# Optimization experiments

Hardware: AMD Instinct MI355X
Metric: run time of the kernel (lower is better)

The kernel has to match this reference:

```python
import jax, jax.numpy as jnp
import numpy as np

# dims: B batch, T spikes, X/Y output grid, IN input neurons (weights rows), H hidden neurons
B, T, X, Y = 16, 128, 16, 16
IN_DIM, H_DIM = 256, 64


def setup_inputs() -> dict:
    key = jax.random.key(0)
    k1, k2, k3, k4, k5 = jax.random.split(key, 5)
    inp = {}
    # input only determines batch size in the custom forward (used by backward in torch)
    inp["input"] = jax.random.uniform(k1, (B, IN_DIM, X, Y), jnp.float32) + 0.01
    inp["spikes"] = jax.random.randint(k2, (B, T, X, Y), 0, IN_DIM)
    inp["epsilon_xy"] = jax.random.uniform(k3, (IN_DIM, X, Y), jnp.float32) * 0.1 + 0.01
    inp["epsilon_t_0"] = jax.random.uniform(k4, (T,), jnp.float32) * 0.5 + 0.5
    inp["weights"] = jax.random.uniform(k5, (IN_DIM, H_DIM), jnp.float32) + 1e-3
    inp["h_initial"] = jnp.ones((H_DIM,), jnp.float32) / H_DIM
    inp["forgetting_offset"] = jnp.ones((1,), jnp.float32)
    return inp


def _sbs_hdynamics(spikes, epsilon_xy, epsilon_t_0, weights, h_initial, fo):
    # spikes: [B,T,X,Y] int; weights: [IN,H]; epsilon_xy: [IN,X,Y]; h_initial: [H]
    b, t, x, y = spikes.shape
    h = weights.shape[1]
    xg = jnp.arange(x)[None, :, None]  # broadcast index grids for [B,X,Y] gathers
    yg = jnp.arange(y)[None, None, :]
    fo_per_neuron = fo / h
    h0 = jnp.broadcast_to(h_initial, (b, x, y, h)).astype(weights.dtype)

    def step(h_state, inp):
        sp, eps_t = inp                      # sp: [B,X,Y], eps_t: scalar
        w = weights[sp]                      # [B,X,Y,H] gather of weight rows
        eps = epsilon_xy[sp, xg, yg] * eps_t # [B,X,Y] per-pixel/spike epsilon
        h_temp = h_state * w                 # [B,X,Y,H]
        s = h_temp.sum(axis=-1)              # [B,X,Y]
        safe_s = jnp.where(s > 1e-10, s, 1.0)
        scale = (eps / safe_s)[..., None]
        # h <- (h + eps*h*w/ (h.w) + eps*fo/H) / (1 + eps*(1+fo))  (fo=0 reduces to h/(1+eps))
        upd = (h_state + scale * h_temp + (eps * fo_per_neuron)[..., None]) / (
            1.0 + (eps * (1.0 + fo))[..., None]
        )
        h_new = jnp.where((s > 1e-10)[..., None], upd, h_state)
        return h_new, None

    spikes_t = jnp.transpose(spikes, (1, 0, 2, 3))  # [T,B,X,Y]
    h_final, _ = jax.lax.scan(step, h0, (spikes_t, epsilon_t_0))
    return jnp.transpose(h_final, (0, 3, 1, 2))  # [B,H,X,Y]


def reference(input, spikes, epsilon_xy, epsilon_t_0, weights, h_initial, forgetting_offset):
    fo = forgetting_offset[0]
    return _sbs_hdynamics(spikes, epsilon_xy, epsilon_t_0, weights, h_initial, fo)
```

## Files before the change

### kernel.cpp

```cpp
#include <hip/hip_runtime.h>

#define BB      16
#define TT      128
#define XDIM    16
#define YDIM    16
#define IN_DIM  256
#define H_DIM   64
#define XY      (XDIM*YDIM)


#define DPP_ADD(v, ctrl)                                                      \
    v += __int_as_float(__builtin_amdgcn_update_dpp(                          \
        0, __float_as_int(v), (ctrl), 0xf, 0xf, true))

#define STEP(W, RD, ERD)                                                      \
    {                                                                         \
        const float ht0 = h.x * (W).x;                                        \
        const float ht1 = h.y * (W).y;                                        \
        const float ht2 = h.z * (W).z;                                        \
        const float ht3 = h.w * (W).w;                                        \
        float r = (ht0 + ht1) + (ht2 + ht3);                                  \
        const float erdf = (ERD) * fo_h;                                      \
        const float eht0 = (ERD) * ht0;                                       \
        const float eht1 = (ERD) * ht1;                                       \
        const float eht2 = (ERD) * ht2;                                       \
        const float eht3 = (ERD) * ht3;                                       \
        const float t30 = fmaf(h.x, (RD), erdf);                              \
        const float t31 = fmaf(h.y, (RD), erdf);                              \
        const float t32 = fmaf(h.z, (RD), erdf);                              \
        const float t33 = fmaf(h.w, (RD), erdf);                              \
        DPP_ADD(r, 0xB1);                                 \
        DPP_ADD(r, 0x4E);                    \
        DPP_ADD(r, 0x124);                                     \
        DPP_ADD(r, 0x128);                 \
        const float rs = __builtin_amdgcn_rcpf(r);  \
        h.x = fmaf(rs, eht0, t30);                                            \
        h.y = fmaf(rs, eht1, t31);                                            \
        h.z = fmaf(rs, eht2, t32);                                            \
        h.w = fmaf(rs, eht3, t33);                                            \
    }

__global__ __launch_bounds__(256) void sbs_scan_kernel(
    const int*   __restrict__ spikes,
    const float* __restrict__ eps_xy,
    const float* __restrict__ eps_t,
    const float* __restrict__ weights,
    const float* __restrict__ h_init,
    const float* __restrict__ fo_ptr,
    float*       __restrict__ out)
{
    __shared__ int4   s_spk4[YDIM][TT / 4 + 1];
    __shared__ float4 s_P4[YDIM][TT / 2 + 1];
    __shared__ float  s_out[YDIM][H_DIM + 1];

    const int tid = threadIdx.x;
    const int bi  = blockIdx.x;
    const int b   = bi >> 4;
    const int x   = bi & 15;

    int spv[8];
    #pragma unroll
    for (int k = 0; k < 8; ++k) {
        const int idx = tid + k * 256;
        const int t = idx >> 4, yy = idx & 15;
        const int sp = spikes[(b * TT + t) * XY + x * YDIM + yy];
        spv[k] = sp;
        ((int*)s_spk4[yy])[t] = sp;
    }

    const float fo   = fo_ptr[0];
    const float fo1  = 1.0f + fo;
    const float fo_h = fo * (1.0f / (float)H_DIM);

    #pragma unroll
    for (int k = 0; k < 8; ++k) {
        const int idx = tid + k * 256;
        const int t = idx >> 4, yy = idx & 15;
        const float eps = eps_xy[spv[k] * XY + x * YDIM + yy] * eps_t[t];
        const float den = fmaf(eps, fo1, 1.0f);
        float rd = __builtin_amdgcn_rcpf(den);
        rd = fmaf(rd, fmaf(-den, rd, 1.0f), rd);
        ((float2*)s_P4[yy])[t] = make_float2(rd, eps * rd);
    }
    __syncthreads();

    const int wave = tid >> 6;
    const int lane = tid & 63;
    const int row  = lane >> 4;
    const int il   = lane & 15;
    const int y    = wave * 4 + row;

    const float4* __restrict__ w4 = (const float4*)weights;
    const int4*   __restrict__ Sy = s_spk4[y];
    const float4* __restrict__ Py = s_P4[y];

    float4 h = ((const float4*)h_init)[il];

    const int4 s0 = Sy[0];
    int4   sA  = Sy[1];
    int4   sB  = Sy[2];
    float4 wq0 = w4[s0.x * 16 + il];
    float4 wq1 = w4[s0.y * 16 + il];
    float4 wq2 = w4[s0.z * 16 + il];
    float4 wq3 = w4[s0.w * 16 + il];
    float4 PA0 = Py[0], PA1 = Py[1];
    float4 PB0 = Py[2], PB1 = Py[3];

    #pragma unroll 2
    for (int g = 0; g < TT / 4; ++g) {
        const int4   s_in  = Sy[(g + 3) & 31];
        const float4 p_in0 = Py[(2 * g + 4) & 63];
        const float4 p_in1 = Py[(2 * g + 5) & 63];
        const float4 wn0 = w4[sA.x * 16 + il];
        const float4 wn1 = w4[sA.y * 16 + il];
        const float4 wn2 = w4[sA.z * 16 + il];
        const float4 wn3 = w4[sA.w * 16 + il];

        STEP(wq0, PA0.x, PA0.y);
        STEP(wq1, PA0.z, PA0.w);
        STEP(wq2, PA1.x, PA1.y);
        STEP(wq3, PA1.z, PA1.w);

        wq0 = wn0; wq1 = wn1; wq2 = wn2; wq3 = wn3;
        PA0 = PB0; PA1 = PB1; PB0 = p_in0; PB1 = p_in1;
        sA = sB; sB = s_in;
    }

    *(float4*)&s_out[y][4 * il] = h;
    __syncthreads();
    #pragma unroll
    for (int k = 0; k < 4; ++k) {
        const int idx = tid + k * 256;
        const int hh = idx >> 4, yy = idx & 15;
        out[b * (H_DIM * XY) + hh * XY + x * YDIM + yy] = s_out[yy][hh];
    }
}

extern "C" void kernel_launch(void* const* d_in, const int* in_sizes, int n_in,
                              void* d_out, int out_size, void* d_ws, size_t ws_size,
                              hipStream_t stream) {
    const int*   spikes  = (const int*)  d_in[1];
    const float* eps_xy  = (const float*)d_in[2];
    const float* eps_t   = (const float*)d_in[3];
    const float* weights = (const float*)d_in[4];
    const float* h_init  = (const float*)d_in[5];
    const float* fo_ptr  = (const float*)d_in[6];
    float*       out     = (float*)d_out;

    const int grid = BB * XDIM;
    sbs_scan_kernel<<<grid, 256, 0, stream>>>(
        spikes, eps_xy, eps_t, weights, h_init, fo_ptr, out);
}
```

Measured before the change: 76.96 us.

## Split each pixel's hidden vector across 32 lanes to double grid parallelism

Each pixel's 64-element hidden state is now spread over 32 lanes holding two values each, where before it was 16 lanes holding four. The per-step dot product therefore needs a cross-half-wave reduction, done with permlane32_swap when available and a shuffle otherwise. Each block now handles 8 pixels, so the grid doubles from 256 to 512 blocks. The aim is to cut the length of each lane's serial recurrence and fill more CUs on the MI355X, at the cost of an extra cross-lane reduction on the critical path of every timestep.

```diff
diff --git a/kernel.cpp b/kernel.cpp
--- a/kernel.cpp
+++ b/kernel.cpp
@@ -13,31 +13,34 @@
     v += __int_as_float(__builtin_amdgcn_update_dpp(                          \
         0, __float_as_int(v), (ctrl), 0xf, 0xf, true))
 
+__device__ __forceinline__ float cross_half_sum(float r) {
+#if __has_builtin(__builtin_amdgcn_permlane32_swap)
+    auto res = __builtin_amdgcn_permlane32_swap(
+        __float_as_uint(r), __float_as_uint(r), false, false);
+    return __uint_as_float(res[0]) + __uint_as_float(res[1]);
+#else
+    return r + __shfl_xor(r, 32);
+#endif
+}
+
 #define STEP(W, RD, ERD)                                                      \
     {                                                                         \
         const float ht0 = h.x * (W).x;                                        \
         const float ht1 = h.y * (W).y;                                        \
-        const float ht2 = h.z * (W).z;                                        \
-        const float ht3 = h.w * (W).w;                                        \
-        float r = (ht0 + ht1) + (ht2 + ht3);                                  \
+        float r = ht0 + ht1;                                                  \
         const float erdf = (ERD) * fo_h;                                      \
         const float eht0 = (ERD) * ht0;                                       \
         const float eht1 = (ERD) * ht1;                                       \
-        const float eht2 = (ERD) * ht2;                                       \
-        const float eht3 = (ERD) * ht3;                                       \
         const float t30 = fmaf(h.x, (RD), erdf);                              \
         const float t31 = fmaf(h.y, (RD), erdf);                              \
-        const float t32 = fmaf(h.z, (RD), erdf);                              \
-        const float t33 = fmaf(h.w, (RD), erdf);                              \
         DPP_ADD(r, 0xB1);                                 \
         DPP_ADD(r, 0x4E);                    \
         DPP_ADD(r, 0x124);                                     \
-        DPP_ADD(r, 0x128);                 \
-        const float rs = __builtin_amdgcn_rcpf(r);  \
+        DPP_ADD(r, 0x128);          \
+        const float s = cross_half_sum(r);        \
+        const float rs = __builtin_amdgcn_rcpf(s);  \
         h.x = fmaf(rs, eht0, t30);                                            \
         h.y = fmaf(rs, eht1, t31);                                            \
-        h.z = fmaf(rs, eht2, t32);                                            \
-        h.w = fmaf(rs, eht3, t33);                                            \
     }
 
 __global__ __launch_bounds__(256) void sbs_scan_kernel(
@@ -49,23 +52,24 @@
     const float* __restrict__ fo_ptr,
     float*       __restrict__ out)
 {
-    __shared__ int4   s_spk4[YDIM][TT / 4 + 1];
-    __shared__ float4 s_P4[YDIM][TT / 2 + 1];
-    __shared__ float  s_out[YDIM][H_DIM + 1];
+    __shared__ int4   s_spk4[8][TT / 4 + 1];
+    __shared__ float4 s_P4[8][TT / 2 + 1];
+    __shared__ float  s_out[8][H_DIM + 1];
 
     const int tid = threadIdx.x;
     const int bi  = blockIdx.x;
-    const int b   = bi >> 4;
-    const int x   = bi & 15;
+    const int b   = bi >> 5;
+    const int x   = (bi >> 1) & 15;
+    const int y0  = (bi & 1) * 8;
 
-    int spv[8];
+    int spv[4];
     #pragma unroll
-    for (int k = 0; k < 8; ++k) {
+    for (int k = 0; k < 4; ++k) {
         const int idx = tid + k * 256;
-        const int t = idx >> 4, yy = idx & 15;
-        const int sp = spikes[(b * TT + t) * XY + x * YDIM + yy];
+        const int t = idx >> 3, pb = idx & 7;
+        const int sp = spikes[(b * TT + t) * XY + x * YDIM + y0 + pb];
         spv[k] = sp;
-        ((int*)s_spk4[yy])[t] = sp;
+        ((int*)s_spk4[pb])[t] = sp;
     }
 
     const float fo   = fo_ptr[0];
@@ -73,36 +77,36 @@
     const float fo_h = fo * (1.0f / (float)H_DIM);
 
     #pragma unroll
-    for (int k = 0; k < 8; ++k) {
+    for (int k = 0; k < 4; ++k) {
         const int idx = tid + k * 256;
-        const int t = idx >> 4, yy = idx & 15;
-        const float eps = eps_xy[spv[k] * XY + x * YDIM + yy] * eps_t[t];
+        const int t = idx >> 3, pb = idx & 7;
+        const float eps = eps_xy[spv[k] * XY + x * YDIM + y0 + pb] * eps_t[t];
         const float den = fmaf(eps, fo1, 1.0f);
         float rd = __builtin_amdgcn_rcpf(den);
         rd = fmaf(rd, fmaf(-den, rd, 1.0f), rd);
-        ((float2*)s_P4[yy])[t] = make_float2(rd, eps * rd);
+        ((float2*)s_P4[pb])[t] = make_float2(rd, eps * rd);
     }
     __syncthreads();
 
     const int wave = tid >> 6;
     const int lane = tid & 63;
-    const int row  = lane >> 4;
-    const int il   = lane & 15;
-    const int y    = wave * 4 + row;
+    const int p    = (lane >> 4) & 1;
+    const int pb   = wave * 2 + p;
+    const int ip   = (lane & 15) | ((lane >> 5) << 4);
 
-    const float4* __restrict__ w4 = (const float4*)weights;
-    const int4*   __restrict__ Sy = s_spk4[y];
-    const float4* __restrict__ Py = s_P4[y];
+    const float2* __restrict__ w2 = (const float2*)weights;
+    const int4*   __restrict__ Sy = s_spk4[pb];
+    const float4* __restrict__ Py = s_P4[pb];
 
-    float4 h = ((const float4*)h_init)[il];
+    float2 h = ((const float2*)h_init)[ip];
 
     const int4 s0 = Sy[0];
     int4   sA  = Sy[1];
     int4   sB  = Sy[2];
-    float4 wq0 = w4[s0.x * 16 + il];
-    float4 wq1 = w4[s0.y * 16 + il];
-    float4 wq2 = w4[s0.z * 16 + il];
-    float4 wq3 = w4[s0.w * 16 + il];
+    float2 wq0 = w2[s0.x * 32 + ip];
+    float2 wq1 = w2[s0.y * 32 + ip];
+    float2 wq2 = w2[s0.z * 32 + ip];
+    float2 wq3 = w2[s0.w * 32 + ip];
     float4 PA0 = Py[0], PA1 = Py[1];
     float4 PB0 = Py[2], PB1 = Py[3];
 
@@ -111,10 +115,10 @@
         const int4   s_in  = Sy[(g + 3) & 31];
         const float4 p_in0 = Py[(2 * g + 4) & 63];
         const float4 p_in1 = Py[(2 * g + 5) & 63];
-        const float4 wn0 = w4[sA.x * 16 + il];
-        const float4 wn1 = w4[sA.y * 16 + il];
-        const float4 wn2 = w4[sA.z * 16 + il];
-        const float4 wn3 = w4[sA.w * 16 + il];
+        const float2 wn0 = w2[sA.x * 32 + ip];
+        const float2 wn1 = w2[sA.y * 32 + ip];
+        const float2 wn2 = w2[sA.z * 32 + ip];
+        const float2 wn3 = w2[sA.w * 32 + ip];
 
         STEP(wq0, PA0.x, PA0.y);
         STEP(wq1, PA0.z, PA0.w);
@@ -126,13 +130,13 @@
         sA = sB; sB = s_in;
     }
 
-    *(float4*)&s_out[y][4 * il] = h;
+    *(float2*)&s_out[pb][2 * ip] = h;
     __syncthreads();
     #pragma unroll
-    for (int k = 0; k < 4; ++k) {
+    for (int k = 0; k < 2; ++k) {
         const int idx = tid + k * 256;
-        const int hh = idx >> 4, yy = idx & 15;
-        out[b * (H_DIM * XY) + hh * XY + x * YDIM + yy] = s_out[yy][hh];
+        const int hh = idx >> 3, p2 = idx & 7;
+        out[b * (H_DIM * XY) + hh * XY + x * YDIM + y0 + p2] = s_out[p2][hh];
     }
 }
 
@@ -147,7 +151,7 @@
     const float* fo_ptr  = (const float*)d_in[6];
     float*       out     = (float*)d_out;
 
-    const int grid = BB * XDIM;
+    const int grid = BB * XDIM * (YDIM / 8);
     sbs_scan_kernel<<<grid, 256, 0, stream>>>(
         spikes, eps_xy, eps_t, weights, h_init, fo_ptr, out);
 }
```

New measurement: 79.86 us. 1.04x slower.
